# Kernel tuning notes

Hardware: AMD Instinct MI355X
Metric: run time of the kernel (lower is better)

The kernel has to match this reference:

```python
import jax, jax.numpy as jnp
import numpy as np


def setup_inputs() -> dict:
    key = jax.random.key(0)
    ks = jax.random.split(key, 5)
    B, S, C, H = 32, 512, 320, 512
    scale = 1.0 / np.sqrt(H)
    return {
        "x": jax.random.normal(ks[0], (B, S, C), dtype=jnp.float32),
        "w_ih": jax.random.normal(ks[1], (4 * H, S), dtype=jnp.float32) * scale,
        "w_hh": jax.random.normal(ks[2], (4 * H, H), dtype=jnp.float32) * scale,
        "b_ih": jax.random.normal(ks[3], (4 * H,), dtype=jnp.float32) * scale,
        "b_hh": jax.random.normal(ks[4], (4 * H,), dtype=jnp.float32) * scale,
    }


def reference(x, w_ih, w_hh, b_ih, b_hh):
    # x: (B, S, C). Original permutes to (B, C, S) and runs a length-1 LSTM per
    # channel with zero initial state -> single LSTM cell step:
    #   gates = x_c @ W_ih^T + b_ih + b_hh   (W_hh @ h0 == 0)
    # PyTorch gate order: i, f, g, o.
    B, S, C = x.shape
    H = w_hh.shape[1]
    gates = jnp.einsum("bsc,gs->bcg", x, w_ih) + b_ih + b_hh  # (B, C, 4H)
    i_g, f_g, g_g, o_g = jnp.split(gates, 4, axis=-1)
    c = jax.nn.sigmoid(i_g) * jnp.tanh(g_g)           # c0 = 0
    h = jax.nn.sigmoid(o_g) * jnp.tanh(c)             # (B, C, H)
    # Faithful to torch: cat over channels along batch dim -> (C*B, H),
    # then reshape to (B, C, H) (scrambles batch/channel order).
    h = jnp.transpose(h, (1, 0, 2)).reshape(B, C, H)
    # dropout is identity in eval mode
    return jnp.transpose(h, (0, 2, 1))                # (B, H, C)
```

## Files before the change

kernel.cpp:

```cpp
#include <hip/hip_runtime.h>
#include <stdint.h>

#define B_  32
#define S_  512
#define C_  320
#define H_  512
#define NROW (B_*C_)

typedef __attribute__((ext_vector_type(8))) short short8;
typedef __attribute__((ext_vector_type(4))) float f32x4;

__device__ __forceinline__ unsigned short f2bf(float x){
  unsigned u = __builtin_bit_cast(unsigned, x);
  u = u + 0x7FFFu + ((u >> 16) & 1u);
  return (unsigned short)(u >> 16);
}
__device__ __forceinline__ float bf2f(unsigned short h){
  unsigned u = ((unsigned)h) << 16;
  return __builtin_bit_cast(float, u);
}
__device__ __forceinline__ float sigf(float x){ return 1.0f/(1.0f + __expf(-x)); }
__device__ __forceinline__ float tanh_fast(float x){ return 2.0f/(1.0f + __expf(-2.0f*x)) - 1.0f; }

__device__ __forceinline__ void gload16(const void* g, void* l){
  __builtin_amdgcn_global_load_lds((const __attribute__((address_space(1))) void*)g,
                                   (__attribute__((address_space(3))) void*)l, 16, 0, 0);
}

__global__ __launch_bounds__(256) void k_cast_w(const float* __restrict__ w,
                                                unsigned short* __restrict__ aws){
  int flat = blockIdx.x*256 + threadIdx.x;
  int plane = flat >> 16;
  int rem   = flat & 65535;
  int srow  = (plane == 0 ? 0 : (plane == 1 ? 1024 : 1536));
  float4 v = ((const float4*)w)[srow*128 + rem];
  uint2 p;
  p.x = (unsigned)f2bf(v.x) | ((unsigned)f2bf(v.y) << 16);
  p.y = (unsigned)f2bf(v.z) | ((unsigned)f2bf(v.w) << 16);
  ((uint2*)aws)[flat] = p;
}

__global__ __launch_bounds__(256) void k_cast_tx(const float* __restrict__ x,
                                                 unsigned short* __restrict__ xws){
  __shared__ float lds[64][65];
  const int tid = threadIdx.x;
  const int st = blockIdx.x, ctt = blockIdx.y, b = blockIdx.z;
  const int s0 = st*64, c0 = ctt*64;
  const int row = tid >> 2, q = tid & 3;

  const float* src = x + ((size_t)(b*S_ + s0 + row))*C_ + c0 + q*16;
  #pragma unroll
  for (int j = 0; j < 4; j++){
    float4 v = ((const float4*)src)[j];
    lds[row][q*16 + j*4 + 0] = v.x;
    lds[row][q*16 + j*4 + 1] = v.y;
    lds[row][q*16 + j*4 + 2] = v.z;
    lds[row][q*16 + j*4 + 3] = v.w;
  }
  __syncthreads();
  const int crow = row;
  #pragma unroll
  for (int j = 0; j < 2; j++){
    short8 o;
    #pragma unroll
    for (int e = 0; e < 8; e++)
      o[e] = (short)f2bf(lds[q*16 + j*8 + e][crow]);
    *(short8*)(xws + ((size_t)(b*C_ + c0 + crow))*S_ + s0 + q*16 + j*8) = o;
  }
}

__global__ __launch_bounds__(256, 3) void k_gemm(const unsigned short* __restrict__ aws,
                                                 const unsigned short* __restrict__ xws,
                                                 const float* __restrict__ b_ih,
                                                 const float* __restrict__ b_hh,
                                                 unsigned short* __restrict__ hws){
  __shared__ alignas(16) char lds[40960];

  const int tid  = threadIdx.x;
  const int w    = tid >> 6;
  const int lane = tid & 63;
  const int wm = w >> 1, wn = w & 1;

  const int bid = blockIdx.x;
  const int x8 = bid & 7, y = bid >> 3;
  const int kt = y & 7, n2 = y >> 3;
  const int nt = n2*8 + x8;
  const int k0 = kt*64;
  const int nbase = nt*128;

  f32x4 acc[3][2][4];
  #pragma unroll
  for (int gi = 0; gi < 3; gi++)
    #pragma unroll
    for (int mf = 0; mf < 2; mf++)
      #pragma unroll
      for (int nf = 0; nf < 4; nf++)
        acc[gi][mf][nf] = (f32x4){0.f, 0.f, 0.f, 0.f};

  const int cr   = lane >> 3;
  const int slot = ((lane & 7) ^ cr) << 4;

  const char* wsb = (const char*)aws;
  unsigned srcoff[10];
  int      dstoff[10];
  #pragma unroll
  for (int i = 0; i < 10; i++){
    int q = w*10 + i;
    if (q < 24){
      int gi = q >> 3, q8 = q & 7;
      int grow = gi*512 + k0 + q8*8 + cr;
      srcoff[i] = (unsigned)(grow*1024 + slot);
      dstoff[i] = gi*8192 + q8*1024;
    } else {
      int q8 = q - 24;
      int xrow = nbase + q8*8 + cr;
      srcoff[i] = (unsigned)(2097152 + xrow*1024 + slot);
      dstoff[i] = 24576 + q8*1024;
    }
  }

  const int lo16 = (lane >> 4) << 4;
  const int swz  = (lane & 7) << 4;
  const int l15  = lane & 15;

  for (int t = 0; t < 8; t++){
    #pragma unroll
    for (int i = 0; i < 10; i++){
      gload16(wsb + (size_t)srcoff[i], &lds[0] + dstoff[i]);
      srcoff[i] += 128;
    }
    __syncthreads();
    #pragma unroll
    for (int ks = 0; ks < 2; ks++){
      const int colb = (ks*64 + lo16) ^ swz;
      short8 aF[3][2], bF[4];
      #pragma unroll
      for (int gi = 0; gi < 3; gi++)
        #pragma unroll
        for (int mf = 0; mf < 2; mf++)
          aF[gi][mf] = *(const short8*)(&lds[0] + gi*8192 + (wm*32 + mf*16 + l15)*128 + colb);
      #pragma unroll
      for (int nf = 0; nf < 4; nf++)
        bF[nf] = *(const short8*)(&lds[0] + 24576 + (wn*64 + nf*16 + l15)*128 + colb);
      #pragma unroll
      for (int gi = 0; gi < 3; gi++)
        #pragma unroll
        for (int mf = 0; mf < 2; mf++)
          #pragma unroll
          for (int nf = 0; nf < 4; nf++)
            acc[gi][mf][nf] = __builtin_amdgcn_mfma_f32_16x16x32_bf16(aF[gi][mf], bF[nf], acc[gi][mf][nf], 0, 0, 0);
    }
    __syncthreads();
  }

  #pragma unroll
  for (int mf = 0; mf < 2; mf++){
    const int kb = k0 + wm*32 + mf*16 + ((lane >> 4) << 2);
    float bi[4], bg[4], bo[4];
    #pragma unroll
    for (int r = 0; r < 4; r++){
      bi[r] = b_ih[kb + r]        + b_hh[kb + r];
      bg[r] = b_ih[1024 + kb + r] + b_hh[1024 + kb + r];
      bo[r] = b_ih[1536 + kb + r] + b_hh[1536 + kb + r];
    }
    #pragma unroll
    for (int nf = 0; nf < 4; nf++){
      const int n = nbase + wn*64 + nf*16 + l15;
      const int bb = n / 320;
      const int cc = n - bb*320;
      const size_t nr = (size_t)cc*32 + (size_t)bb;
      float h[4];
      #pragma unroll
      for (int r = 0; r < 4; r++){
        float iv = acc[0][mf][nf][r] + bi[r];
        float gv = acc[1][mf][nf][r] + bg[r];
        float ov = acc[2][mf][nf][r] + bo[r];
        float ce = sigf(iv) * tanh_fast(gv);
        h[r] = sigf(ov) * tanh_fast(ce);
      }
      uint2 p2;
      p2.x = (unsigned)f2bf(h[0]) | ((unsigned)f2bf(h[1]) << 16);
      p2.y = (unsigned)f2bf(h[2]) | ((unsigned)f2bf(h[3]) << 16);
      *(uint2*)(hws + nr*H_ + kb) = p2;
    }
  }
}

__global__ __launch_bounds__(256) void k_out(const unsigned short* __restrict__ hws,
                                             float* __restrict__ out){
  __shared__ float lds[64][65];
  const int tid = threadIdx.x;
  const int kt = blockIdx.x, ctt = blockIdx.y, b2 = blockIdx.z;
  const int k0 = kt*64, n0 = b2*320 + ctt*64;
  const int rr = tid >> 2, q = tid & 3;

  #pragma unroll
  for (int j = 0; j < 2; j++){
    short8 v = *(const short8*)(hws + ((size_t)(n0 + rr))*H_ + k0 + q*16 + j*8);
    #pragma unroll
    for (int e = 0; e < 8; e++)
      lds[rr][q*16 + j*8 + e] = bf2f((unsigned short)v[e]);
  }
  __syncthreads();
  const int krow = rr;
  #pragma unroll
  for (int j = 0; j < 4; j++){
    int c2l = q*16 + j*4;
    float4 o;
    o.x = lds[c2l + 0][krow];
    o.y = lds[c2l + 1][krow];
    o.z = lds[c2l + 2][krow];
    o.w = lds[c2l + 3][krow];
    *(float4*)(out + (size_t)b2*(H_*C_) + (size_t)(k0 + krow)*C_ + ctt*64 + c2l) = o;
  }
}

extern "C" void kernel_launch(void* const* d_in, const int* in_sizes, int n_in,
                              void* d_out, int out_size, void* d_ws, size_t ws_size,
                              hipStream_t stream){
  const float* x    = (const float*)d_in[0];
  const float* w_ih = (const float*)d_in[1];
  const float* b_ih = (const float*)d_in[3];
  const float* b_hh = (const float*)d_in[4];
  float* out = (float*)d_out;

  char* ws = (char*)d_ws;
  unsigned short* aws = (unsigned short*)(ws);
  unsigned short* xws = (unsigned short*)(ws + 2097152);
  unsigned short* hws = (unsigned short*)(ws + 2097152 + 10485760);

  k_cast_w <<<768, 256, 0, stream>>>(w_ih, aws);
  k_cast_tx<<<dim3(8, 5, 32), 256, 0, stream>>>(x, xws);
  k_gemm   <<<640, 256, 0, stream>>>(aws, xws, b_ih, b_hh, hws);
  k_out    <<<dim3(8, 5, 32), 256, 0, stream>>>(hws, out);
}
```

Before: 55.58 us.

## Double-buffer GEMM LDS via register prefetch and merge cast kernels

The GEMM swaps direct global-to-LDS loads for register-staged loads into a double-buffered LDS tile. The next k-slice is fetched while MFMAs run on the current one, which drops one barrier per iteration. LDS use doubles, so launch bounds fall from 3 to 2 blocks per CU, costing occupancy. The weight-cast and x-transpose kernels are also merged into one launch to save launch overhead.

```diff
diff --git a/kernel.cpp b/kernel.cpp
--- a/kernel.cpp
+++ b/kernel.cpp
@@ -22,29 +22,29 @@
 __device__ __forceinline__ float sigf(float x){ return 1.0f/(1.0f + __expf(-x)); }
 __device__ __forceinline__ float tanh_fast(float x){ return 2.0f/(1.0f + __expf(-2.0f*x)) - 1.0f; }
 
-__device__ __forceinline__ void gload16(const void* g, void* l){
-  __builtin_amdgcn_global_load_lds((const __attribute__((address_space(1))) void*)g,
-                                   (__attribute__((address_space(3))) void*)l, 16, 0, 0);
-}
-
-__global__ __launch_bounds__(256) void k_cast_w(const float* __restrict__ w,
-                                                unsigned short* __restrict__ aws){
-  int flat = blockIdx.x*256 + threadIdx.x;
-  int plane = flat >> 16;
-  int rem   = flat & 65535;
-  int srow  = (plane == 0 ? 0 : (plane == 1 ? 1024 : 1536));
-  float4 v = ((const float4*)w)[srow*128 + rem];
-  uint2 p;
-  p.x = (unsigned)f2bf(v.x) | ((unsigned)f2bf(v.y) << 16);
-  p.y = (unsigned)f2bf(v.z) | ((unsigned)f2bf(v.w) << 16);
-  ((uint2*)aws)[flat] = p;
-}
-
-__global__ __launch_bounds__(256) void k_cast_tx(const float* __restrict__ x,
-                                                 unsigned short* __restrict__ xws){
+__global__ __launch_bounds__(256) void k_prep(const float* __restrict__ w,
+                                              const float* __restrict__ x,
+                                              unsigned short* __restrict__ aws,
+                                              unsigned short* __restrict__ xws){
+  const int bidg = blockIdx.x;
+  const int tid = threadIdx.x;
+  if (bidg < 768){
+    int flat = bidg*256 + tid;
+    int plane = flat >> 16;
+    int rem   = flat & 65535;
+    int srow  = (plane == 0 ? 0 : (plane == 1 ? 1024 : 1536));
+    float4 v = ((const float4*)w)[srow*128 + rem];
+    uint2 p;
+    p.x = (unsigned)f2bf(v.x) | ((unsigned)f2bf(v.y) << 16);
+    p.y = (unsigned)f2bf(v.z) | ((unsigned)f2bf(v.w) << 16);
+    ((uint2*)aws)[flat] = p;
+    return;
+  }
   __shared__ float lds[64][65];
-  const int tid = threadIdx.x;
-  const int st = blockIdx.x, ctt = blockIdx.y, b = blockIdx.z;
+  const int idx = bidg - 768;
+  const int st = idx & 7;
+  const int r5 = idx >> 3;
+  const int ctt = r5 % 5, b = r5 / 5;
   const int s0 = st*64, c0 = ctt*64;
   const int row = tid >> 2, q = tid & 3;
 
@@ -69,12 +69,12 @@
   }
 }
 
-__global__ __launch_bounds__(256, 3) void k_gemm(const unsigned short* __restrict__ aws,
+__global__ __launch_bounds__(256, 2) void k_gemm(const unsigned short* __restrict__ aws,
                                                  const unsigned short* __restrict__ xws,
                                                  const float* __restrict__ b_ih,
                                                  const float* __restrict__ b_hh,
                                                  unsigned short* __restrict__ hws){
-  __shared__ alignas(16) char lds[40960];
+  __shared__ alignas(16) char lds[2][40960];
 
   const int tid  = threadIdx.x;
   const int w    = tid >> 6;
@@ -110,26 +110,41 @@
       int gi = q >> 3, q8 = q & 7;
       int grow = gi*512 + k0 + q8*8 + cr;
       srcoff[i] = (unsigned)(grow*1024 + slot);
-      dstoff[i] = gi*8192 + q8*1024;
+      dstoff[i] = gi*8192 + q8*1024 + (lane << 4);
     } else {
       int q8 = q - 24;
       int xrow = nbase + q8*8 + cr;
       srcoff[i] = (unsigned)(2097152 + xrow*1024 + slot);
-      dstoff[i] = 24576 + q8*1024;
-    }
-  }
+      dstoff[i] = 24576 + q8*1024 + (lane << 4);
+    }
+  }
+
+  short8 ld[10];
+  #pragma unroll
+  for (int i = 0; i < 10; i++)
+    ld[i] = *(const short8*)(wsb + (size_t)srcoff[i]);
+  #pragma unroll
+  for (int i = 0; i < 10; i++)
+    *(short8*)(&lds[0][0] + dstoff[i]) = ld[i];
+  __syncthreads();
 
   const int lo16 = (lane >> 4) << 4;
   const int swz  = (lane & 7) << 4;
   const int l15  = lane & 15;
 
+  #pragma unroll
   for (int t = 0; t < 8; t++){
-    #pragma unroll
-    for (int i = 0; i < 10; i++){
-      gload16(wsb + (size_t)srcoff[i], &lds[0] + dstoff[i]);
-      srcoff[i] += 128;
-    }
-    __syncthreads();
+    const int p = t & 1;
+    char* base  = &lds[0][0] + p*40960;
+    char* other = &lds[0][0] + (p^1)*40960;
+
+    if (t < 7){
+      #pragma unroll
+      for (int i = 0; i < 10; i++)
+        ld[i] = *(const short8*)(wsb + (size_t)(srcoff[i] + (unsigned)(t+1)*128));
+      __builtin_amdgcn_sched_barrier(0);
+    }
+
     #pragma unroll
     for (int ks = 0; ks < 2; ks++){
       const int colb = (ks*64 + lo16) ^ swz;
@@ -138,10 +153,10 @@
       for (int gi = 0; gi < 3; gi++)
         #pragma unroll
         for (int mf = 0; mf < 2; mf++)
-          aF[gi][mf] = *(const short8*)(&lds[0] + gi*8192 + (wm*32 + mf*16 + l15)*128 + colb);
+          aF[gi][mf] = *(const short8*)(base + gi*8192 + (wm*32 + mf*16 + l15)*128 + colb);
       #pragma unroll
       for (int nf = 0; nf < 4; nf++)
-        bF[nf] = *(const short8*)(&lds[0] + 24576 + (wn*64 + nf*16 + l15)*128 + colb);
+        bF[nf] = *(const short8*)(base + 24576 + (wn*64 + nf*16 + l15)*128 + colb);
       #pragma unroll
       for (int gi = 0; gi < 3; gi++)
         #pragma unroll
@@ -149,6 +164,12 @@
           #pragma unroll
           for (int nf = 0; nf < 4; nf++)
             acc[gi][mf][nf] = __builtin_amdgcn_mfma_f32_16x16x32_bf16(aF[gi][mf], bF[nf], acc[gi][mf][nf], 0, 0, 0);
+    }
+
+    if (t < 7){
+      #pragma unroll
+      for (int i = 0; i < 10; i++)
+        *(short8*)(other + dstoff[i]) = ld[i];
     }
     __syncthreads();
   }
@@ -229,8 +250,7 @@
   unsigned short* xws = (unsigned short*)(ws + 2097152);
   unsigned short* hws = (unsigned short*)(ws + 2097152 + 10485760);
 
-  k_cast_w <<<768, 256, 0, stream>>>(w_ih, aws);
-  k_cast_tx<<<dim3(8, 5, 32), 256, 0, stream>>>(x, xws);
-  k_gemm   <<<640, 256, 0, stream>>>(aws, xws, b_ih, b_hh, hws);
-  k_out    <<<dim3(8, 5, 32), 256, 0, stream>>>(hws, out);
-}
+  k_prep <<<2048, 256, 0, stream>>>(w_ih, x, aws, xws);
+  k_gemm <<<640, 256, 0, stream>>>(aws, xws, b_ih, b_hh, hws);
+  k_out  <<<dim3(8, 5, 32), 256, 0, stream>>>(hws, out);
+}
```

New measurement: 53.57 us. 3.6% less time.

## Fuse output transpose into GEMM epilogue and merge cast kernels

Applied to the files above, without the earlier changes.

Merges the weight-cast and x-transpose-cast kernels into a single launch, and stores x rows pre-permuted into the scrambled (c*32+b) order. The GEMM epilogue then stages fp32 h tiles in LDS and writes the final transposed output directly, removing the bf16 h intermediate round trip and the separate output-transpose kernel. It also raises the occupancy hint in launch bounds from 3 to 4. The cost is extra LDS traffic and a barrier in the epilogue, plus possible register pressure under the tighter bound.

```diff
diff --git a/kernel.cpp b/kernel.cpp
--- a/kernel.cpp
+++ b/kernel.cpp
@@ -15,10 +15,6 @@
   u = u + 0x7FFFu + ((u >> 16) & 1u);
   return (unsigned short)(u >> 16);
 }
-__device__ __forceinline__ float bf2f(unsigned short h){
-  unsigned u = ((unsigned)h) << 16;
-  return __builtin_bit_cast(float, u);
-}
 __device__ __forceinline__ float sigf(float x){ return 1.0f/(1.0f + __expf(-x)); }
 __device__ __forceinline__ float tanh_fast(float x){ return 2.0f/(1.0f + __expf(-2.0f*x)) - 1.0f; }
 
@@ -27,24 +23,29 @@
                                    (__attribute__((address_space(3))) void*)l, 16, 0, 0);
 }
 
-__global__ __launch_bounds__(256) void k_cast_w(const float* __restrict__ w,
-                                                unsigned short* __restrict__ aws){
-  int flat = blockIdx.x*256 + threadIdx.x;
-  int plane = flat >> 16;
-  int rem   = flat & 65535;
-  int srow  = (plane == 0 ? 0 : (plane == 1 ? 1024 : 1536));
-  float4 v = ((const float4*)w)[srow*128 + rem];
-  uint2 p;
-  p.x = (unsigned)f2bf(v.x) | ((unsigned)f2bf(v.y) << 16);
-  p.y = (unsigned)f2bf(v.z) | ((unsigned)f2bf(v.w) << 16);
-  ((uint2*)aws)[flat] = p;
-}
-
-__global__ __launch_bounds__(256) void k_cast_tx(const float* __restrict__ x,
-                                                 unsigned short* __restrict__ xws){
+__global__ __launch_bounds__(256) void k_prep(const float* __restrict__ w,
+                                              const float* __restrict__ x,
+                                              unsigned short* __restrict__ aws,
+                                              unsigned short* __restrict__ xws){
+  const int bidg = blockIdx.x;
+  const int tid = threadIdx.x;
+  if (bidg < 768){
+    int flat = bidg*256 + tid;
+    int plane = flat >> 16;
+    int rem   = flat & 65535;
+    int srow  = (plane == 0 ? 0 : (plane == 1 ? 1024 : 1536));
+    float4 v = ((const float4*)w)[srow*128 + rem];
+    uint2 p;
+    p.x = (unsigned)f2bf(v.x) | ((unsigned)f2bf(v.y) << 16);
+    p.y = (unsigned)f2bf(v.z) | ((unsigned)f2bf(v.w) << 16);
+    ((uint2*)aws)[flat] = p;
+    return;
+  }
   __shared__ float lds[64][65];
-  const int tid = threadIdx.x;
-  const int st = blockIdx.x, ctt = blockIdx.y, b = blockIdx.z;
+  const int idx = bidg - 768;
+  const int st = idx & 7;
+  const int r5 = idx >> 3;
+  const int ctt = r5 % 5, b = r5 / 5;
   const int s0 = st*64, c0 = ctt*64;
   const int row = tid >> 2, q = tid & 3;
 
@@ -59,21 +60,22 @@
   }
   __syncthreads();
   const int crow = row;
+  const size_t nprime = (size_t)(c0 + crow)*32 + (size_t)b;
   #pragma unroll
   for (int j = 0; j < 2; j++){
     short8 o;
     #pragma unroll
     for (int e = 0; e < 8; e++)
       o[e] = (short)f2bf(lds[q*16 + j*8 + e][crow]);
-    *(short8*)(xws + ((size_t)(b*C_ + c0 + crow))*S_ + s0 + q*16 + j*8) = o;
-  }
-}
-
-__global__ __launch_bounds__(256, 3) void k_gemm(const unsigned short* __restrict__ aws,
+    *(short8*)(xws + nprime*S_ + s0 + q*16 + j*8) = o;
+  }
+}
+
+__global__ __launch_bounds__(256, 4) void k_gemm(const unsigned short* __restrict__ aws,
                                                  const unsigned short* __restrict__ xws,
                                                  const float* __restrict__ b_ih,
                                                  const float* __restrict__ b_hh,
-                                                 unsigned short* __restrict__ hws){
+                                                 float* __restrict__ out){
   __shared__ alignas(16) char lds[40960];
 
   const int tid  = threadIdx.x;
@@ -153,22 +155,22 @@
     __syncthreads();
   }
 
+  float* tr = (float*)&lds[0];
   #pragma unroll
   for (int mf = 0; mf < 2; mf++){
-    const int kb = k0 + wm*32 + mf*16 + ((lane >> 4) << 2);
+    const int kl = wm*32 + mf*16 + ((lane >> 4) << 2);
+    const int kg = k0 + kl;
     float bi[4], bg[4], bo[4];
     #pragma unroll
     for (int r = 0; r < 4; r++){
-      bi[r] = b_ih[kb + r]        + b_hh[kb + r];
-      bg[r] = b_ih[1024 + kb + r] + b_hh[1024 + kb + r];
-      bo[r] = b_ih[1536 + kb + r] + b_hh[1536 + kb + r];
+      bi[r] = b_ih[kg + r]        + b_hh[kg + r];
+      bg[r] = b_ih[1024 + kg + r] + b_hh[1024 + kg + r];
+      bo[r] = b_ih[1536 + kg + r] + b_hh[1536 + kg + r];
     }
     #pragma unroll
     for (int nf = 0; nf < 4; nf++){
-      const int n = nbase + wn*64 + nf*16 + l15;
-      const int bb = n / 320;
-      const int cc = n - bb*320;
-      const size_t nr = (size_t)cc*32 + (size_t)bb;
+      const int nl = wn*64 + nf*16 + l15;
+      float4 hv;
       float h[4];
       #pragma unroll
       for (int r = 0; r < 4; r++){
@@ -178,40 +180,27 @@
         float ce = sigf(iv) * tanh_fast(gv);
         h[r] = sigf(ov) * tanh_fast(ce);
       }
-      uint2 p2;
-      p2.x = (unsigned)f2bf(h[0]) | ((unsigned)f2bf(h[1]) << 16);
-      p2.y = (unsigned)f2bf(h[2]) | ((unsigned)f2bf(h[3]) << 16);
-      *(uint2*)(hws + nr*H_ + kb) = p2;
-    }
-  }
-}
-
-__global__ __launch_bounds__(256) void k_out(const unsigned short* __restrict__ hws,
-                                             float* __restrict__ out){
-  __shared__ float lds[64][65];
-  const int tid = threadIdx.x;
-  const int kt = blockIdx.x, ctt = blockIdx.y, b2 = blockIdx.z;
-  const int k0 = kt*64, n0 = b2*320 + ctt*64;
-  const int rr = tid >> 2, q = tid & 3;
-
-  #pragma unroll
-  for (int j = 0; j < 2; j++){
-    short8 v = *(const short8*)(hws + ((size_t)(n0 + rr))*H_ + k0 + q*16 + j*8);
-    #pragma unroll
-    for (int e = 0; e < 8; e++)
-      lds[rr][q*16 + j*8 + e] = bf2f((unsigned short)v[e]);
+      hv.x = h[0]; hv.y = h[1]; hv.z = h[2]; hv.w = h[3];
+      *(float4*)(tr + nl*68 + kl) = hv;
+    }
   }
   __syncthreads();
-  const int krow = rr;
-  #pragma unroll
-  for (int j = 0; j < 4; j++){
-    int c2l = q*16 + j*4;
-    float4 o;
-    o.x = lds[c2l + 0][krow];
-    o.y = lds[c2l + 1][krow];
-    o.z = lds[c2l + 2][krow];
-    o.w = lds[c2l + 3][krow];
-    *(float4*)(out + (size_t)b2*(H_*C_) + (size_t)(k0 + krow)*C_ + ctt*64 + c2l) = o;
+
+  const int ko  = tid >> 2;
+  const int sub = tid & 3;
+  const size_t krow_off = (size_t)(k0 + ko)*C_;
+  #pragma unroll
+  for (int jj = 0; jj < 8; jj++){
+    const int nl = sub*32 + jj*4;
+    const int ng = nbase + nl;
+    const int b2 = ng / 320;
+    const int c2 = ng - b2*320;
+    float4 v;
+    v.x = tr[(nl+0)*68 + ko];
+    v.y = tr[(nl+1)*68 + ko];
+    v.z = tr[(nl+2)*68 + ko];
+    v.w = tr[(nl+3)*68 + ko];
+    *(float4*)(out + (size_t)b2*(H_*C_) + krow_off + c2) = v;
   }
 }
 
@@ -227,10 +216,7 @@
   char* ws = (char*)d_ws;
   unsigned short* aws = (unsigned short*)(ws);
   unsigned short* xws = (unsigned short*)(ws + 2097152);
-  unsigned short* hws = (unsigned short*)(ws + 2097152 + 10485760);
-
-  k_cast_w <<<768, 256, 0, stream>>>(w_ih, aws);
-  k_cast_tx<<<dim3(8, 5, 32), 256, 0, stream>>>(x, xws);
-  k_gemm   <<<640, 256, 0, stream>>>(aws, xws, b_ih, b_hh, hws);
-  k_out    <<<dim3(8, 5, 32), 256, 0, stream>>>(hws, out);
-}
+
+  k_prep <<<2048, 256, 0, stream>>>(w_ih, x, aws, xws);
+  k_gemm <<<640, 256, 0, stream>>>(aws, xws, b_ih, b_hh, out);
+}
```

Result: no change. 54.89 us (-1.2%).
